# Performance work log

Measured on AMD Instinct MI355X. Metric: run time of the kernel, lower is better.

Reference implementation:

```python
import jax, jax.numpy as jnp
import numpy as np

N_DRUG = 846
D = 256          # embedding_num
K = 128          # neighbor_sample_size
N_REL = 200
N_ENT = 100000
BN_EPS = 1e-5


def setup_inputs() -> dict:
    key = jax.random.key(0)
    ks = jax.random.split(key, 12)
    drug_name = jnp.arange(N_DRUG, dtype=jnp.int64) if jax.config.jax_enable_x64 else jnp.arange(N_DRUG, dtype=jnp.int32)
    adj_tail = jax.random.randint(ks[0], (N_DRUG, K), 0, N_ENT)
    adj_relation = jax.random.randint(ks[1], (N_DRUG, K), 0, N_REL)
    drug_table = jax.random.normal(ks[2], (N_DRUG, D), dtype=jnp.float32)
    rela_table = jax.random.normal(ks[3], (N_REL, D), dtype=jnp.float32)
    ent_table = jax.random.normal(ks[4], (N_ENT, D), dtype=jnp.float32)
    W1 = jax.random.normal(ks[5], (N_DRUG, D, D), dtype=jnp.float32) * 0.05
    b1 = jax.random.normal(ks[6], (K, D), dtype=jnp.float32) * 0.05
    W2 = jax.random.normal(ks[7], (N_DRUG, D, D), dtype=jnp.float32) * 0.05
    b2 = jax.random.normal(ks[8], (K, D), dtype=jnp.float32) * 0.05
    # Linear(2D -> D), xavier-uniform weight, zero bias
    lim = np.sqrt(6.0 / (2 * D + D)).astype(np.float32)
    lin_w = jax.random.uniform(ks[9], (D, 2 * D), minval=-lim, maxval=lim, dtype=jnp.float32)
    lin_b = jnp.zeros((D,), dtype=jnp.float32)
    bn_gamma = jnp.ones((D,), dtype=jnp.float32)
    bn_beta = jnp.zeros((D,), dtype=jnp.float32)
    return {
        "drug_name": drug_name, "adj_tail": adj_tail, "adj_relation": adj_relation,
        "drug_table": drug_table, "rela_table": rela_table, "ent_table": ent_table,
        "W1": W1, "b1": b1, "W2": W2, "b2": b2,
        "lin_w": lin_w, "lin_b": lin_b, "bn_gamma": bn_gamma, "bn_beta": bn_beta,
    }


def reference(drug_name, adj_tail, adj_relation, drug_table, rela_table, ent_table,
              W1, b1, W2, b2, lin_w, lin_b, bn_gamma, bn_beta):
    drug_emb = drug_table[drug_name]                  # [N, D]
    rela_emb = rela_table[adj_relation]               # [N, K, D]
    ent_emb = ent_table[adj_tail]                     # [N, K, D]

    drug_rel = drug_emb[:, None, :] * rela_emb        # [N, K, D]
    h = jnp.einsum('nkd,nde->nke', drug_rel, W1) + b1 # per-drug bmm + bias
    h = jax.nn.relu(h)
    h = jnp.einsum('nkd,nde->nke', h, W2) + b2        # [N, K, D]

    score = jnp.sum(h, axis=-1, keepdims=True)        # [N, K, 1]
    score = jax.nn.softmax(score, axis=1)             # softmax over neighbors

    weighted_ent = jnp.einsum('nk,nkd->nd', score[..., 0], ent_emb)  # [N, D]
    drug_e = jnp.concatenate([weighted_ent, drug_emb], axis=1)       # [N, 2D]

    x = drug_e @ lin_w.T + lin_b                      # Linear(2D -> D)
    x = jax.nn.relu(x)
    # BatchNorm1d in training mode: biased batch statistics
    mean = jnp.mean(x, axis=0)
    var = jnp.var(x, axis=0)
    drug_f = bn_gamma * (x - mean) * jax.lax.rsqrt(var + BN_EPS) + bn_beta
    return drug_f
```

## Files before the change

### kernel.cpp

```cpp
#include <hip/hip_runtime.h>
#include <math.h>

#define NDRUG 846
#define DIM   256
#define KN    128

typedef _Float16 half8 __attribute__((ext_vector_type(8)));
typedef float f32x4 __attribute__((ext_vector_type(4)));

__global__ __launch_bounds__(256) void b2sum_kernel(const float* __restrict__ b2,
                                                    float* __restrict__ b2sum) {
    int row  = blockIdx.x * 4 + (threadIdx.x >> 6);
    int lane = threadIdx.x & 63;
    if (row >= KN) return;
    float4 v = *((const float4*)(b2 + (size_t)row * DIM) + lane);
    float s = v.x + v.y + v.z + v.w;
    #pragma unroll
    for (int off = 32; off >= 1; off >>= 1) s += __shfl_xor(s, off);
    if (lane == 0) b2sum[row] = s;
}

__global__ __launch_bounds__(256) void w2sum_kernel(const float* __restrict__ W2,
                                                    float* __restrict__ w2s) {
    const int nrows = NDRUG * DIM;
    const int nw    = (gridDim.x * 256) >> 6;
    const int wid   = (blockIdx.x * 256 + threadIdx.x) >> 6;
    const int lane  = threadIdx.x & 63;
    for (int r = wid; r < nrows; r += nw) {
        float4 v = *((const float4*)(W2 + (size_t)r * DIM) + lane);
        float s = (v.x + v.y) + (v.z + v.w);
        #pragma unroll
        for (int off = 32; off >= 1; off >>= 1) s += __shfl_xor(s, off);
        if (lane == 0) w2s[r] = s;
    }
}

__global__ __launch_bounds__(256, 2) void gnn_main(
    const int* __restrict__ adj_rel,
    const float* __restrict__ drug_table, const float* __restrict__ rela_table,
    const float* __restrict__ W1, const float* __restrict__ b1,
    const float* __restrict__ b2sum, const float* __restrict__ w2s,
    float* __restrict__ score_out)
{
    __shared__ __align__(16) half8 sB[8][8][64];
    __shared__ __align__(16) _Float16 sA[2][4][520];
    __shared__ __align__(16) float s_drug[DIM];
    __shared__ float s_w2[DIM];
    __shared__ int   s_ridx[KN];
    __shared__ float s_scoreP[4][KN];
    __shared__ float s_red[8];

    const int n    = blockIdx.x;
    const int t    = threadIdx.x;
    const int wv   = t >> 6;
    const int lane = t & 63;

    const float* W1n   = W1 + (size_t)n * DIM * DIM;
    const float* wbase = W1n + (size_t)(wv << 3) * DIM + lane;
    float PA[8], PB[8];
    {
        #pragma unroll
        for (int j = 0; j < 8; ++j) PA[j] = wbase[(size_t)j * DIM];
        const float* p1 = wbase + (size_t)32 * DIM;
        #pragma unroll
        for (int j = 0; j < 8; ++j) PB[j] = p1[(size_t)j * DIM];
    }

    s_drug[t] = drug_table[(size_t)n * DIM + t];
    s_w2[t]   = w2s[(size_t)n * DIM + t];
    float sc_init = 0.f;
    if (t < KN) { s_ridx[t] = adj_rel[(size_t)n * KN + t]; sc_init = b2sum[t]; }
    __syncthreads();

    {
        const int kk = t >> 1, o0 = (t & 1) << 1;
        const float* rrow = rela_table + (size_t)s_ridx[kk] * DIM;
        #pragma unroll 2
        for (int s8 = 0; s8 < 8; ++s8) {
            #pragma unroll
            for (int i = 0; i < 2; ++i) {
                const int o  = o0 | i;
                const int db = (s8 << 5) + (o << 3);
                float4 p0 = *(const float4*)(rrow + db);
                float4 p1 = *(const float4*)(rrow + db + 4);
                float4 q0 = *(const float4*)(s_drug + db);
                float4 q1 = *(const float4*)(s_drug + db + 4);
                half8 h;
                h[0] = (_Float16)(p0.x * q0.x);
                h[1] = (_Float16)(p0.y * q0.y);
                h[2] = (_Float16)(p0.z * q0.z);
                h[3] = (_Float16)(p0.w * q0.w);
                h[4] = (_Float16)(p1.x * q1.x);
                h[5] = (_Float16)(p1.y * q1.y);
                h[6] = (_Float16)(p1.z * q1.z);
                h[7] = (_Float16)(p1.w * q1.w);
                sB[s8][kk >> 4][(kk & 15) | (o << 4)] = h;
            }
        }
    }

    const int kcol = lane & 15, quad = lane >> 4;
    f32x4 acc[8] = {};
    float sacc[8] = {0.f,0.f,0.f,0.f,0.f,0.f,0.f,0.f};
    const f32x4 fzero = {};

    auto step = [&](int ss, float (&P)[8]) {
        half8 hw;
        #pragma unroll
        for (int j = 0; j < 8; ++j) hw[j] = (_Float16)P[j];
        *(half8*)&sA[ss & 1][lane >> 4][((lane & 15) | (wv << 4)) << 3] = hw;
        if (ss + 2 < 32) {
            const float* p = wbase + (size_t)(((ss + 2) & 7) << 5) * DIM
                                   + (((ss + 2) >> 3) << 6);
            #pragma unroll
            for (int j = 0; j < 8; ++j) P[j] = p[(size_t)j * DIM];
        }
        asm volatile("s_waitcnt lgkmcnt(0)\n\ts_barrier" ::: "memory");
        half8 af = *(const half8*)&sA[ss & 1][wv][(size_t)lane << 3];
        const int ds = ss & 7;
        #pragma unroll
        for (int kt = 0; kt < 8; ++kt) {
            half8 bf = sB[ds][kt][lane];
            acc[kt] = __builtin_amdgcn_mfma_f32_16x16x32_f16(af, bf, acc[kt], 0, 0, 0);
        }
        if (ds == 7) {
            const int c = ss >> 3;
            const int ebase = (c << 6) + (wv << 4) + (quad << 2);
            float4 ww = *(const float4*)(s_w2 + ebase);
            #pragma unroll
            for (int kt = 0; kt < 8; ++kt) {
                const int k = (kt << 4) + kcol;
                float4 bb = *(const float4*)(b1 + (size_t)k * DIM + ebase);
                f32x4 a = acc[kt];
                sacc[kt] += fmaxf(a[0] + bb.x, 0.f) * ww.x
                          + fmaxf(a[1] + bb.y, 0.f) * ww.y
                          + fmaxf(a[2] + bb.z, 0.f) * ww.z
                          + fmaxf(a[3] + bb.w, 0.f) * ww.w;
                acc[kt] = fzero;
            }
        }
    };
    for (int sp = 0; sp < 16; ++sp) { step(2 * sp, PA); step(2 * sp + 1, PB); }

    #pragma unroll
    for (int kt = 0; kt < 8; ++kt) {
        float v = sacc[kt];
        v += __shfl_xor(v, 16);
        v += __shfl_xor(v, 32);
        if (lane < 16) s_scoreP[wv][(kt << 4) + lane] = v;
    }
    __syncthreads();
    float sc = -3.0e38f;
    if (t < KN)
        sc = sc_init + (s_scoreP[0][t] + s_scoreP[1][t]) + (s_scoreP[2][t] + s_scoreP[3][t]);

    float mx = sc;
    #pragma unroll
    for (int off = 32; off >= 1; off >>= 1) mx = fmaxf(mx, __shfl_xor(mx, off));
    if (lane == 0) s_red[wv] = mx;
    __syncthreads();
    float M = fmaxf(fmaxf(s_red[0], s_red[1]), fmaxf(s_red[2], s_red[3]));
    float ex = (t < KN) ? expf(sc - M) : 0.f;
    float ssum = ex;
    #pragma unroll
    for (int off = 32; off >= 1; off >>= 1) ssum += __shfl_xor(ssum, off);
    if (lane == 0) s_red[4 + wv] = ssum;
    __syncthreads();
    float S = (s_red[4] + s_red[5]) + (s_red[6] + s_red[7]);
    if (t < KN) score_out[(size_t)n * KN + t] = ex / S;
}

__global__ __launch_bounds__(256) void gather_kernel(
    const float* __restrict__ score, const int* __restrict__ adj_tail,
    const float* __restrict__ ent_table, const float* __restrict__ drug_table,
    float* __restrict__ drug_e)
{
    __shared__ float s_p[KN];
    __shared__ int   s_ti[KN];
    const int n = blockIdx.x, t = threadIdx.x;
    if (t < KN) {
        s_p[t]  = score[(size_t)n * KN + t];
        s_ti[t] = adj_tail[(size_t)n * KN + t];
    }
    __syncthreads();
    float a0=0.f,a1=0.f,a2=0.f,a3=0.f,a4=0.f,a5=0.f,a6=0.f,a7=0.f;
    for (int k = 0; k < KN; k += 8) {
        float v0 = ent_table[(size_t)s_ti[k + 0] * DIM + t];
        float v1 = ent_table[(size_t)s_ti[k + 1] * DIM + t];
        float v2 = ent_table[(size_t)s_ti[k + 2] * DIM + t];
        float v3 = ent_table[(size_t)s_ti[k + 3] * DIM + t];
        float v4 = ent_table[(size_t)s_ti[k + 4] * DIM + t];
        float v5 = ent_table[(size_t)s_ti[k + 5] * DIM + t];
        float v6 = ent_table[(size_t)s_ti[k + 6] * DIM + t];
        float v7 = ent_table[(size_t)s_ti[k + 7] * DIM + t];
        a0 += s_p[k + 0] * v0;  a1 += s_p[k + 1] * v1;
        a2 += s_p[k + 2] * v2;  a3 += s_p[k + 3] * v3;
        a4 += s_p[k + 4] * v4;  a5 += s_p[k + 5] * v5;
        a6 += s_p[k + 6] * v6;  a7 += s_p[k + 7] * v7;
    }
    drug_e[(size_t)n * 512 + t]       = ((a0 + a1) + (a2 + a3)) + ((a4 + a5) + (a6 + a7));
    drug_e[(size_t)n * 512 + DIM + t] = drug_table[(size_t)n * DIM + t];
}

__global__ __launch_bounds__(256) void linear_kernel(
    const float* __restrict__ drug_e, const float* __restrict__ lin_w,
    const float* __restrict__ lin_b,
    float* __restrict__ x, float* __restrict__ g_sum, float* __restrict__ g_sumsq)
{
    __shared__ __align__(16) float s_de[4][512];
    const int b = blockIdx.x, t = threadIdx.x;
    const int n0 = b * 4;
    #pragma unroll
    for (int ss = 0; ss < 2; ++ss) {
        int idx = ss * 256 + t;
        int row = idx >> 7, col4 = idx & 127;
        float4 v = make_float4(0.f, 0.f, 0.f, 0.f);
        if (n0 + row < NDRUG) v = *((const float4*)(drug_e + (size_t)(n0 + row) * 512) + col4);
        *(float4*)&s_de[row][col4 * 4] = v;
    }
    __syncthreads();
    float acc[4] = {};
    const float4* wrow = (const float4*)(lin_w + (size_t)t * 512);
    #pragma unroll 4
    for (int d4 = 0; d4 < 128; ++d4) {
        float4 w = wrow[d4];
        #pragma unroll
        for (int i = 0; i < 4; ++i) {
            float4 de = *(const float4*)&s_de[i][d4 * 4];
            acc[i] += w.x * de.x + w.y * de.y + w.z * de.z + w.w * de.w;
        }
    }
    float bias = lin_b[t];
    float psum = 0.f, psq = 0.f;
    #pragma unroll
    for (int i = 0; i < 4; ++i) {
        if (n0 + i < NDRUG) {
            float v = fmaxf(acc[i] + bias, 0.f);
            x[(size_t)(n0 + i) * DIM + t] = v;
            psum += v; psq += v * v;
        }
    }
    atomicAdd(&g_sum[t], psum);
    atomicAdd(&g_sumsq[t], psq);
}

__global__ __launch_bounds__(256) void bn_kernel(
    const float* __restrict__ x, const float* __restrict__ g_sum,
    const float* __restrict__ g_sumsq,
    const float* __restrict__ gamma, const float* __restrict__ beta,
    float* __restrict__ out)
{
    const int n = blockIdx.x, e = threadIdx.x;
    const float inv = 1.0f / (float)NDRUG;
    float mean = g_sum[e] * inv;
    float var  = fmaxf(g_sumsq[e] * inv - mean * mean, 0.f);
    float rstd = rsqrtf(var + 1e-5f);
    float v = x[(size_t)n * DIM + e];
    out[(size_t)n * DIM + e] = gamma[e] * (v - mean) * rstd + beta[e];
}

extern "C" void kernel_launch(void* const* d_in, const int* in_sizes, int n_in,
                              void* d_out, int out_size, void* d_ws, size_t ws_size,
                              hipStream_t stream) {
    const int*   adj_tail   = (const int*)d_in[1];
    const int*   adj_rel    = (const int*)d_in[2];
    const float* drug_table = (const float*)d_in[3];
    const float* rela_table = (const float*)d_in[4];
    const float* ent_table  = (const float*)d_in[5];
    const float* W1         = (const float*)d_in[6];
    const float* b1         = (const float*)d_in[7];
    const float* W2         = (const float*)d_in[8];
    const float* b2         = (const float*)d_in[9];
    const float* lin_w      = (const float*)d_in[10];
    const float* lin_b      = (const float*)d_in[11];
    const float* gamma      = (const float*)d_in[12];
    const float* beta       = (const float*)d_in[13];
    float* out = (float*)d_out;

    float* ws      = (float*)d_ws;
    float* b2sum   = ws;
    float* drug_e  = ws + 128;
    float* w2s     = drug_e;
    float* xbuf    = drug_e + (size_t)NDRUG * 512;
    float* score_w = xbuf;
    float* g_sum   = xbuf + (size_t)NDRUG * DIM;
    float* g_sumsq = g_sum + DIM;

    hipMemsetAsync(g_sum, 0, 2 * DIM * sizeof(float), stream);
    b2sum_kernel<<<KN / 4, 256, 0, stream>>>(b2, b2sum);
    w2sum_kernel<<<2048, 256, 0, stream>>>(W2, w2s);
    gnn_main<<<NDRUG, 256, 0, stream>>>(adj_rel, drug_table, rela_table,
                                        W1, b1, b2sum, w2s, score_w);
    gather_kernel<<<NDRUG, 256, 0, stream>>>(score_w, adj_tail, ent_table,
                                             drug_table, drug_e);
    linear_kernel<<<(NDRUG + 3) / 4, 256, 0, stream>>>(drug_e, lin_w, lin_b,
                                                       xbuf, g_sum, g_sumsq);
    bn_kernel<<<NDRUG, 256, 0, stream>>>(xbuf, g_sum, g_sumsq, gamma, beta, out);
}
```

Measured before the change: 555.9 us.

## Fuse W2 row-sum into main kernel with deeper four-stage prefetch

Drops the separate w2sum kernel. Each gnn_main block now streams its own W2 slice alongside W1 and reduces the rows with wave shuffles into shared memory, just ahead of the epilogue that uses them. The W1 register prefetch deepens from two stages to four, and the loop is fully unrolled. Drug and relation-index values are read straight from global memory instead of being staged in shared memory, which removes a block barrier. This saves one launch and the w2s write and reread, and exposes more memory parallelism. The cost is much higher register pressure under launch bounds of 256 threads with 2 blocks per unit, plus extra shuffle work in the inner loop.

```diff
diff --git a/kernel.cpp b/kernel.cpp
--- a/kernel.cpp
+++ b/kernel.cpp
@@ -20,33 +20,16 @@
     if (lane == 0) b2sum[row] = s;
 }
 
-__global__ __launch_bounds__(256) void w2sum_kernel(const float* __restrict__ W2,
-                                                    float* __restrict__ w2s) {
-    const int nrows = NDRUG * DIM;
-    const int nw    = (gridDim.x * 256) >> 6;
-    const int wid   = (blockIdx.x * 256 + threadIdx.x) >> 6;
-    const int lane  = threadIdx.x & 63;
-    for (int r = wid; r < nrows; r += nw) {
-        float4 v = *((const float4*)(W2 + (size_t)r * DIM) + lane);
-        float s = (v.x + v.y) + (v.z + v.w);
-        #pragma unroll
-        for (int off = 32; off >= 1; off >>= 1) s += __shfl_xor(s, off);
-        if (lane == 0) w2s[r] = s;
-    }
-}
-
 __global__ __launch_bounds__(256, 2) void gnn_main(
     const int* __restrict__ adj_rel,
     const float* __restrict__ drug_table, const float* __restrict__ rela_table,
     const float* __restrict__ W1, const float* __restrict__ b1,
-    const float* __restrict__ b2sum, const float* __restrict__ w2s,
+    const float* __restrict__ W2, const float* __restrict__ b2sum,
     float* __restrict__ score_out)
 {
     __shared__ __align__(16) half8 sB[8][8][64];
     __shared__ __align__(16) _Float16 sA[2][4][520];
-    __shared__ __align__(16) float s_drug[DIM];
     __shared__ float s_w2[DIM];
-    __shared__ int   s_ridx[KN];
     __shared__ float s_scoreP[4][KN];
     __shared__ float s_red[8];
 
@@ -56,25 +39,28 @@
     const int lane = t & 63;
 
     const float* W1n   = W1 + (size_t)n * DIM * DIM;
+    const float* W2n   = W2 + (size_t)n * DIM * DIM;
     const float* wbase = W1n + (size_t)(wv << 3) * DIM + lane;
-    float PA[8], PB[8];
+    const int w2row0 = (wv << 1) + (lane >> 5);
+    const int w2c    = lane & 31;
+
+    const int kk = t >> 1, o0 = (t & 1) << 1;
+    const int   rid     = adj_rel[(size_t)n * KN + kk];
+    const float sc_init = b2sum[t & (KN - 1)];
+
+    float P[4][8]; float4 Qa[4], Qb[4];
+    #pragma unroll
+    for (int s = 0; s < 4; ++s) {
+        const float* p = wbase + (size_t)((s & 7) << 5) * DIM + ((s >> 3) << 6);
+        #pragma unroll
+        for (int j = 0; j < 8; ++j) P[s][j] = p[(size_t)j * DIM];
+        const float4* wr = (const float4*)(W2n + (size_t)((s << 3) + w2row0) * DIM);
+        Qa[s] = wr[w2c]; Qb[s] = wr[32 + w2c];
+    }
+
     {
-        #pragma unroll
-        for (int j = 0; j < 8; ++j) PA[j] = wbase[(size_t)j * DIM];
-        const float* p1 = wbase + (size_t)32 * DIM;
-        #pragma unroll
-        for (int j = 0; j < 8; ++j) PB[j] = p1[(size_t)j * DIM];
-    }
-
-    s_drug[t] = drug_table[(size_t)n * DIM + t];
-    s_w2[t]   = w2s[(size_t)n * DIM + t];
-    float sc_init = 0.f;
-    if (t < KN) { s_ridx[t] = adj_rel[(size_t)n * KN + t]; sc_init = b2sum[t]; }
-    __syncthreads();
-
-    {
-        const int kk = t >> 1, o0 = (t & 1) << 1;
-        const float* rrow = rela_table + (size_t)s_ridx[kk] * DIM;
+        const float* rrow = rela_table + (size_t)rid * DIM;
+        const float* drow = drug_table + (size_t)n * DIM;
         #pragma unroll 2
         for (int s8 = 0; s8 < 8; ++s8) {
             #pragma unroll
@@ -83,8 +69,8 @@
                 const int db = (s8 << 5) + (o << 3);
                 float4 p0 = *(const float4*)(rrow + db);
                 float4 p1 = *(const float4*)(rrow + db + 4);
-                float4 q0 = *(const float4*)(s_drug + db);
-                float4 q1 = *(const float4*)(s_drug + db + 4);
+                float4 q0 = *(const float4*)(drow + db);
+                float4 q1 = *(const float4*)(drow + db + 4);
                 half8 h;
                 h[0] = (_Float16)(p0.x * q0.x);
                 h[1] = (_Float16)(p0.y * q0.y);
@@ -104,16 +90,30 @@
     float sacc[8] = {0.f,0.f,0.f,0.f,0.f,0.f,0.f,0.f};
     const f32x4 fzero = {};
 
-    auto step = [&](int ss, float (&P)[8]) {
+    #pragma unroll
+    for (int ss = 0; ss < 32; ++ss) {
+        const int rb = ss & 3;
         half8 hw;
         #pragma unroll
-        for (int j = 0; j < 8; ++j) hw[j] = (_Float16)P[j];
+        for (int j = 0; j < 8; ++j) hw[j] = (_Float16)P[rb][j];
         *(half8*)&sA[ss & 1][lane >> 4][((lane & 15) | (wv << 4)) << 3] = hw;
-        if (ss + 2 < 32) {
-            const float* p = wbase + (size_t)(((ss + 2) & 7) << 5) * DIM
-                                   + (((ss + 2) >> 3) << 6);
+        {
+            float4 qa = Qa[rb], qb = Qb[rb];
+            float wsum = (qa.x + qa.y + qa.z + qa.w) + (qb.x + qb.y + qb.z + qb.w);
+            wsum += __shfl_xor(wsum, 1);
+            wsum += __shfl_xor(wsum, 2);
+            wsum += __shfl_xor(wsum, 4);
+            wsum += __shfl_xor(wsum, 8);
+            wsum += __shfl_xor(wsum, 16);
+            if ((lane & 31) == 0) s_w2[(ss << 3) + w2row0] = wsum;
+        }
+        if (ss + 4 < 32) {
+            const int sn = ss + 4;
+            const float* p = wbase + (size_t)((sn & 7) << 5) * DIM + ((sn >> 3) << 6);
             #pragma unroll
-            for (int j = 0; j < 8; ++j) P[j] = p[(size_t)j * DIM];
+            for (int j = 0; j < 8; ++j) P[rb][j] = p[(size_t)j * DIM];
+            const float4* wr = (const float4*)(W2n + (size_t)((sn << 3) + w2row0) * DIM);
+            Qa[rb] = wr[w2c]; Qb[rb] = wr[32 + w2c];
         }
         asm volatile("s_waitcnt lgkmcnt(0)\n\ts_barrier" ::: "memory");
         half8 af = *(const half8*)&sA[ss & 1][wv][(size_t)lane << 3];
@@ -139,8 +139,7 @@
                 acc[kt] = fzero;
             }
         }
-    };
-    for (int sp = 0; sp < 16; ++sp) { step(2 * sp, PA); step(2 * sp + 1, PB); }
+    }
 
     #pragma unroll
     for (int kt = 0; kt < 8; ++kt) {
@@ -280,7 +279,6 @@
     float* ws      = (float*)d_ws;
     float* b2sum   = ws;
     float* drug_e  = ws + 128;
-    float* w2s     = drug_e;
     float* xbuf    = drug_e + (size_t)NDRUG * 512;
     float* score_w = xbuf;
     float* g_sum   = xbuf + (size_t)NDRUG * DIM;
@@ -288,9 +286,8 @@
 
     hipMemsetAsync(g_sum, 0, 2 * DIM * sizeof(float), stream);
     b2sum_kernel<<<KN / 4, 256, 0, stream>>>(b2, b2sum);
-    w2sum_kernel<<<2048, 256, 0, stream>>>(W2, w2s);
     gnn_main<<<NDRUG, 256, 0, stream>>>(adj_rel, drug_table, rela_table,
-                                        W1, b1, b2sum, w2s, score_w);
+                                        W1, b1, W2, b2sum, score_w);
     gather_kernel<<<NDRUG, 256, 0, stream>>>(score_w, adj_tail, ent_table,
                                              drug_table, drug_e);
     linear_kernel<<<(NDRUG + 3) / 4, 256, 0, stream>>>(drug_e, lin_w, lin_b,
```

New measurement: 585.7 us. 1.05x slower.
